# Kernel tuning notes

Measured on AMD Instinct MI355X. Metric: run time of the kernel, lower is better.

Reference implementation:

```python
import jax, jax.numpy as jnp
import numpy as np

D_STATE = 8
D_CONV = 4
DT_RANK = 8
THRESHOLD = 0.5
KPOOL = 3
PAD = (KPOOL - 1) // 2
EPS = 1e-5


def _rmsnorm(x, w):
    return x * jax.lax.rsqrt(jnp.mean(x * x, axis=-1, keepdims=True) + EPS) * w


def _dw_causal_conv(x, w, b):
    # x: (L, T, C), w: (C, 1, K) depthwise causal conv along T
    xt = jnp.transpose(x, (0, 2, 1))  # (L, C, T)
    y = jax.lax.conv_general_dilated(
        xt, w, window_strides=(1,), padding=[(D_CONV - 1, 0)],
        dimension_numbers=('NCH', 'OIH', 'NCH'), feature_group_count=xt.shape[1])
    return jnp.transpose(y, (0, 2, 1)) + b


def _selective_scan(x, delta, A, B, Cm, D):
    # x, delta: (L,T,d); A: (d,n); B, Cm: (L,T,n); D: (d,)
    dA = jnp.exp(delta[..., None] * A)                        # (L,T,d,n)
    dBx = (delta * x)[..., None] * B[:, :, None, :]           # (L,T,d,n)
    def combine(a, b):
        a1, b1 = a
        a2, b2 = b
        return (a2 * a1, a2 * b1 + b2)
    _, h = jax.lax.associative_scan(combine, (dA, dBx), axis=1)
    y = jnp.einsum('ltdn,ltn->ltd', h, Cm)
    return y + x * D


def _mamba_block(x, in_proj, conv_w, conv_b, x_proj_w, dt_proj_w, dt_proj_b,
                 A_log_f, A_log_b, D_f, D_b, out_proj_w, rms_w):
    # single-depth bidirectional (bimamba-v2 style) block, expand=1, residual + RMSNorm
    res = x
    xn = _rmsnorm(x, rms_w)
    xz = xn @ in_proj                       # (L,T,2C)
    xi, z = jnp.split(xz, 2, axis=-1)
    xi = jax.nn.silu(_dw_causal_conv(xi, conv_w, conv_b))
    dbl = xi @ x_proj_w                     # (L,T,dt_rank+2*d_state)
    dt = dbl[..., :DT_RANK]
    Bm = dbl[..., DT_RANK:DT_RANK + D_STATE]
    Cm = dbl[..., DT_RANK + D_STATE:]
    delta = jax.nn.softplus(dt @ dt_proj_w + dt_proj_b)
    A_f = -jnp.exp(A_log_f)
    A_b = -jnp.exp(A_log_b)
    flip = lambda a: a[:, ::-1]
    y_f = _selective_scan(xi, delta, A_f, Bm, Cm, D_f)
    y_b = flip(_selective_scan(flip(xi), flip(delta), A_b, flip(Bm), flip(Cm), D_b))
    y = 0.5 * (y_f + y_b) * jax.nn.silu(z)  # if_devide_out -> average two directions
    return res + y @ out_proj_w


def reference(feats, in_proj, conv_w, conv_b, x_proj_w, dt_proj_w, dt_proj_b,
              A_log_f, A_log_b, D_f, D_b, out_proj_w, rms_w, mlp_w, mlp_b,
              record_len):
    N, C, H, W = feats.shape
    T = H * W
    rec = np.asarray(record_len)  # static ragged group sizes
    ends = np.cumsum(rec)
    starts = ends - rec
    masks = []
    for s0, L in zip(starts.tolist(), rec.tolist()):
        g = feats[s0:s0 + L]                       # (L,C,H,W)
        if L > 1:
            x = g.reshape(L, C, T).transpose(0, 2, 1)  # l c h w -> l (h w) c
            feat = _mamba_block(x, in_proj, conv_w, conv_b, x_proj_w, dt_proj_w,
                                dt_proj_b, A_log_f, A_log_b, D_f, D_b,
                                out_proj_w, rms_w)
            score = jax.nn.sigmoid(feat @ mlp_w + mlp_b)   # (L,T,1)
            ego = jnp.ones((1, T, 1), feats.dtype)
            bs = jnp.concatenate([ego, score[1:]], axis=0)
        else:
            bs = jnp.ones((1, T, 1), feats.dtype)
        bs = bs.transpose(0, 2, 1).reshape(L, 1, H, W)     # l (h w) c -> l c h w
        masks.append(jnp.where(bs > THRESHOLD, 1.0, 0.0).astype(feats.dtype))
    mask = jnp.concatenate(masks, axis=0)                  # (N,1,H,W)
    pooled = jax.lax.reduce_window(
        mask, -jnp.inf, jax.lax.max,
        window_dimensions=(1, 1, KPOOL, KPOOL), window_strides=(1, 1, 1, 1),
        padding=[(0, 0), (0, 0), (PAD, PAD), (PAD, PAD)])
    return pooled


def setup_inputs():
    key = jax.random.key(0)
    ks = jax.random.split(key, 8)
    C, H, W = 128, 96, 96
    record_len = np.array([2, 3, 1, 2, 4], dtype=np.int64)
    N = int(record_len.sum())
    s = 0.05
    A_log = jnp.log(jnp.broadcast_to(
        jnp.arange(1, D_STATE + 1, dtype=jnp.float32), (C, D_STATE)))
    return {
        'feats': jax.random.normal(ks[0], (N, C, H, W), jnp.float32),
        'in_proj': jax.random.normal(ks[1], (C, 2 * C), jnp.float32) * s,
        'conv_w': jax.random.normal(ks[2], (C, 1, D_CONV), jnp.float32) * s,
        'conv_b': jnp.zeros((C,), jnp.float32),
        'x_proj_w': jax.random.normal(ks[3], (C, DT_RANK + 2 * D_STATE), jnp.float32) * s,
        'dt_proj_w': jax.random.normal(ks[4], (DT_RANK, C), jnp.float32) * s,
        'dt_proj_b': jnp.full((C,), 0.1, jnp.float32),
        'A_log_f': A_log,
        'A_log_b': A_log,
        'D_f': jnp.ones((C,), jnp.float32),
        'D_b': jnp.ones((C,), jnp.float32),
        'out_proj_w': jax.random.normal(ks[5], (C, C), jnp.float32) * s,
        'rms_w': jnp.ones((C,), jnp.float32),
        'mlp_w': jax.random.normal(ks[6], (C, 1), jnp.float32) * s,
        'mlp_b': jnp.zeros((1,), jnp.float32),
        'record_len': jnp.asarray(record_len),
    }
```

## Files before the change

### kernel.cpp

```cpp
#include <hip/hip_runtime.h>
#include <cstdint>
#include <cstddef>

#define C_CH 128
#define T_TOK 9216
#define H_IMG 96
#define W_IMG 96
#define NSTATE 8

#define CHUNK 32
#define RHALO 32
#define REGION (CHUNK + 2 * RHALO)

__device__ __forceinline__ float siluf_dev(float x) {
  return x / (1.0f + expf(-x));
}

__device__ __forceinline__ float fast_silu(float x) {
  return __fdividef(x, 1.0f + __expf(-x));
}

__global__ __launch_bounds__(128) void k0_setup(
    const int* __restrict__ rec, int n_groups, int N,
    const float* __restrict__ out_proj_w, const float* __restrict__ mlp_w,
    float* __restrict__ vvec, int* __restrict__ slot)
{
  const int tid = threadIdx.x;
  if (tid == 0) {
    int f = 0, sl = 0;
    for (int g = 0; g < n_groups; ++g) {
      const int L = rec[g];
      slot[f] = -1;
      for (int i = 1; i < L; ++i) slot[f + i] = sl++;
      f += L;
    }
  }
  if (tid < C_CH) {
    float acc = 0.0f;
    for (int j = 0; j < C_CH; ++j) acc += out_proj_w[tid * C_CH + j] * mlp_w[j];
    vvec[tid] = acc;
  }
}

__global__ __launch_bounds__(256, 4) void k1_gemm(
    const float* __restrict__ feats, const float* __restrict__ in_proj,
    const float* __restrict__ rms_w, const float* __restrict__ mlp_w,
    const float* __restrict__ mlp_b, const float* __restrict__ vvec,
    const int* __restrict__ slot,
    float* __restrict__ xipre, float* __restrict__ wbuf,
    float* __restrict__ logit)
{
  __shared__ float Asm[C_CH * 64];
  __shared__ float redA[256], redB[256], irS[64];
  const int f = blockIdx.y;
  const int s = slot[f];
  if (s < 0) return;
  const int m0 = blockIdx.x * 64;
  const int tid = threadIdx.x;

  {
    const int c0 = tid >> 4;
    const int tq = (tid & 15) * 4;
    const float* src = feats + (size_t)f * C_CH * T_TOK + m0 + tq;
    #pragma unroll
    for (int i = 0; i < 8; ++i) {
      const int c = c0 + i * 16;
      const float4 x4 = *(const float4*)(src + (size_t)c * T_TOK);
      *(float4*)&Asm[c * 64 + tq] = x4;
    }
  }
  __syncthreads();
  {
    const int t = tid & 63;
    const int q = tid >> 6;
    float ssum = 0.0f, rm = 0.0f;
    for (int cc = q * 32; cc < q * 32 + 32; ++cc) {
      const float val = Asm[cc * 64 + t];
      ssum += val * val;
      rm += val * mlp_w[cc];
    }
    redA[tid] = ssum; redB[tid] = rm;
  }
  __syncthreads();
  if (tid < 64) {
    const int t = tid;
    const float ssum = redA[t] + redA[t + 64] + redA[t + 128] + redA[t + 192];
    const float rm   = redB[t] + redB[t + 64] + redB[t + 128] + redB[t + 192];
    const float ir = 1.0f / sqrtf(ssum * (1.0f / C_CH) + 1e-5f);
    logit[(size_t)s * T_TOK + m0 + t] = rm + mlp_b[0];
    irS[t] = ir;
  }
  __syncthreads();
  {
    const int t = tid & 63;
    const int q = tid >> 6;
    const float ir = irS[t];
    for (int cc = q * 32; cc < q * 32 + 32; ++cc)
      Asm[cc * 64 + t] = (Asm[cc * 64 + t] * ir) * rms_w[cc];
  }
  __syncthreads();

  const int ti = tid >> 4;
  const int tc = tid & 15;
  for (int chunk = 0; chunk < 4; ++chunk) {
    const int n0 = chunk * 64;
    const float* bp = in_proj + n0 + tc * 4;
    float acc[4][4];
    #pragma unroll
    for (int i = 0; i < 4; ++i)
      #pragma unroll
      for (int j = 0; j < 4; ++j) acc[i][j] = 0.0f;
    #pragma unroll 8
    for (int k = 0; k < C_CH; ++k) {
      const float4 a4 = *(const float4*)&Asm[k * 64 + ti * 4];
      const float4 b4 = *(const float4*)(bp + (size_t)k * 256);
      acc[0][0] += a4.x * b4.x; acc[0][1] += a4.x * b4.y; acc[0][2] += a4.x * b4.z; acc[0][3] += a4.x * b4.w;
      acc[1][0] += a4.y * b4.x; acc[1][1] += a4.y * b4.y; acc[1][2] += a4.y * b4.z; acc[1][3] += a4.y * b4.w;
      acc[2][0] += a4.z * b4.x; acc[2][1] += a4.z * b4.y; acc[2][2] += a4.z * b4.z; acc[2][3] += a4.z * b4.w;
      acc[3][0] += a4.w * b4.x; acc[3][1] += a4.w * b4.y; acc[3][2] += a4.w * b4.z; acc[3][3] += a4.w * b4.w;
    }
    if (chunk < 2) {
      const int cb = n0 + tc * 4;
      #pragma unroll
      for (int i = 0; i < 4; ++i) {
        const int t = m0 + ti * 4 + i;
        float4 o; o.x = acc[i][0]; o.y = acc[i][1]; o.z = acc[i][2]; o.w = acc[i][3];
        *(float4*)&xipre[((size_t)s * T_TOK + t) * C_CH + cb] = o;
      }
    } else {
      const int zc = (chunk - 2) * 64 + tc * 4;
      const float4 v4 = *(const float4*)&vvec[zc];
      #pragma unroll
      for (int i = 0; i < 4; ++i) {
        const int t = m0 + ti * 4 + i;
        float4 o;
        o.x = 0.5f * siluf_dev(acc[i][0]) * v4.x;
        o.y = 0.5f * siluf_dev(acc[i][1]) * v4.y;
        o.z = 0.5f * siluf_dev(acc[i][2]) * v4.z;
        o.w = 0.5f * siluf_dev(acc[i][3]) * v4.w;
        *(float4*)&wbuf[((size_t)s * T_TOK + t) * C_CH + zc] = o;
      }
    }
  }
}

__global__ __launch_bounds__(256, 4) void k2_convproj(
    const float* __restrict__ xipre,
    const float* __restrict__ conv_w, const float* __restrict__ conv_b,
    const float* __restrict__ x_proj_w, const int* __restrict__ slot,
    float* __restrict__ dbl_g)
{
  __shared__ float xibuf[64 * 129];
  const int f = blockIdx.y;
  const int s = slot[f];
  if (s < 0) return;
  const int m0 = blockIdx.x * 64;
  const int tid = threadIdx.x;
  const int c = tid & 127;
  const int half = tid >> 7;
  const size_t rowbase = (size_t)s * T_TOK;
  const float4 cw = *(const float4*)(conv_w + c * 4);
  const float cb = conv_b[c];

  auto ldx = [&](int t) -> float {
    return (t >= 0) ? xipre[(rowbase + t) * C_CH + c] : 0.0f;
  };

  {
    const int t0 = m0 + half * 32;
    float xm1 = ldx(t0 - 1), xm2 = ldx(t0 - 2), xm3 = ldx(t0 - 3);
    #pragma unroll
    for (int i = 0; i < 32; ++i) {
      const float cur = ldx(t0 + i);
      const float sum = cw.x * xm3 + cw.y * xm2 + cw.z * xm1 + cw.w * cur + cb;
      xibuf[(half * 32 + i) * 129 + c] = fast_silu(sum);
      xm3 = xm2; xm2 = xm1; xm1 = cur;
    }
  }
  __syncthreads();
  {
    const int q6 = __builtin_amdgcn_readfirstlane(tid >> 6) * 6;
    const int tok = tid & 63;
    float acc[6] = {0, 0, 0, 0, 0, 0};
    for (int cc = 0; cc < C_CH; ++cc) {
      const float xv = xibuf[tok * 129 + cc];
      #pragma unroll
      for (int jj = 0; jj < 6; ++jj)
        acc[jj] += xv * x_proj_w[cc * 24 + q6 + jj];
    }
    #pragma unroll
    for (int jj = 0; jj < 6; ++jj)
      dbl_g[(rowbase + m0 + tok) * 24 + q6 + jj] = acc[jj];
  }
}

__global__ __launch_bounds__(256, 8) void k3_scan(
    const float* __restrict__ xipre, const float* __restrict__ wbuf,
    const float* __restrict__ dbl_g,
    const float* __restrict__ conv_w, const float* __restrict__ conv_b,
    const float* __restrict__ dt_proj_w, const float* __restrict__ dt_proj_b,
    const float* __restrict__ A_log_f, const float* __restrict__ A_log_b,
    const float* __restrict__ D_f, const float* __restrict__ D_b,
    const int* __restrict__ slot, float* __restrict__ logit)
{
  __shared__ float dbl[REGION * 24];
  const int f = blockIdx.y;
  const int s = slot[f];
  if (s < 0) return;
  const int c0 = blockIdx.x * CHUNK;
  const int r0 = c0 - RHALO;
  const int tid = threadIdx.x;
  const int c = tid & 127;
  const int half = tid >> 7;
  const size_t rowbase = (size_t)s * T_TOK;
  const float4 cw = *(const float4*)(conv_w + c * 4);
  const float cb = conv_b[c];

  auto ldx = [&](int t) -> float {
    return (t >= 0 && t < T_TOK) ? xipre[(rowbase + t) * C_CH + c] : 0.0f;
  };

  {
    const long grow = ((long)rowbase + r0) * 24;
    const int lo  = (r0 < 0) ? (-r0) * 6 : 0;
    const int hi  = (r0 + REGION > T_TOK) ? (T_TOK - r0) * 6 : REGION * 6;
    #pragma unroll
    for (int i = 0; i < 3; ++i) {
      const int idx = tid + i * 256;
      if (idx >= lo && idx < hi)
        *(float4*)&dbl[idx * 4] = *(const float4*)&dbl_g[grow + (long)idx * 4];
    }
  }
  __syncthreads();

  float dw[8], Ac[8];
  const float* Alog = half ? A_log_b : A_log_f;
  #pragma unroll
  for (int r = 0; r < 8; ++r) dw[r] = dt_proj_w[r * C_CH + c];
  #pragma unroll
  for (int n = 0; n < NSTATE; ++n) Ac[n] = -expf(Alog[c * NSTATE + n]);
  const float bias = dt_proj_b[c];
  const float Dd = half ? D_b[c] : D_f[c];
  float h[8] = {0, 0, 0, 0, 0, 0, 0, 0};

  const float a0 = Ac[0];
  int okl = 1;
  #pragma unroll
  for (int n = 1; n < NSTATE; ++n)
    okl &= (fabsf(Ac[n] - (float)(n + 1) * a0) <= 1e-4f * fabsf(Ac[n])) ? 1 : 0;
  const bool fastA = (__all(okl) != 0);

  auto decay8 = [&](float dlt, float* dA) {
    if (fastA) {
      const float e1 = __expf(dlt * a0);
      const float e2 = e1 * e1, e3 = e2 * e1, e4 = e2 * e2;
      dA[0] = e1; dA[1] = e2; dA[2] = e3; dA[3] = e4;
      dA[4] = e4 * e1; dA[5] = e4 * e2; dA[6] = e4 * e3; dA[7] = e4 * e4;
    } else {
      #pragma unroll
      for (int n = 0; n < NSTATE; ++n) dA[n] = __expf(dlt * Ac[n]);
    }
  };

  if (half == 0) {
    const int tb = (r0 < 0) ? 0 : r0;
    const int steps = c0 + CHUNK - tb;
    const int outg0 = (c0 - tb) >> 3;
    const int ng = steps >> 3;
    float xm1 = ldx(tb - 1), xm2 = ldx(tb - 2), xm3 = ldx(tb - 3);
    for (int g = 0; g < ng; ++g) {
      const int t0 = tb + g * 8;
      const bool out = (g >= outg0);
      float pg[8], wg[8];
      #pragma unroll
      for (int j = 0; j < 8; ++j) {
        const size_t gi = (rowbase + t0 + j) * C_CH + c;
        pg[j] = xipre[gi];
        wg[j] = out ? wbuf[gi] : 0.0f;
      }
      #pragma unroll
      for (int j = 0; j < 8; ++j) {
        const int t = t0 + j;
        const int p = t - r0;
        const float cur = pg[j];
        const float sum = cw.x * xm3 + cw.y * xm2 + cw.z * xm1 + cw.w * cur + cb;
        const float xiv = fast_silu(sum);
        xm3 = xm2; xm2 = xm1; xm1 = cur;
        const float4 d0 = *(const float4*)&dbl[p * 24];
        const float4 d1 = *(const float4*)&dbl[p * 24 + 4];
        float pre = bias;
        pre += d0.x * dw[0] + d0.y * dw[1] + d0.z * dw[2] + d0.w * dw[3];
        pre += d1.x * dw[4] + d1.y * dw[5] + d1.z * dw[6] + d1.w * dw[7];
        const float dlt = fmaxf(pre, 0.0f) + __logf(1.0f + __expf(-fabsf(pre)));
        const float u = dlt * xiv;
        const float4 b0 = *(const float4*)&dbl[p * 24 + 8];
        const float4 b1 = *(const float4*)&dbl[p * 24 + 12];
        float dA[8];
        decay8(dlt, dA);
        h[0] = dA[0] * h[0] + u * b0.x;
        h[1] = dA[1] * h[1] + u * b0.y;
        h[2] = dA[2] * h[2] + u * b0.z;
        h[3] = dA[3] * h[3] + u * b0.w;
        h[4] = dA[4] * h[4] + u * b1.x;
        h[5] = dA[5] * h[5] + u * b1.y;
        h[6] = dA[6] * h[6] + u * b1.z;
        h[7] = dA[7] * h[7] + u * b1.w;
        if (out) {
          const float4 cc0 = *(const float4*)&dbl[p * 24 + 16];
          const float4 cc1 = *(const float4*)&dbl[p * 24 + 20];
          float y = xiv * Dd;
          y += h[0] * cc0.x + h[1] * cc0.y + h[2] * cc0.z + h[3] * cc0.w;
          y += h[4] * cc1.x + h[5] * cc1.y + h[6] * cc1.z + h[7] * cc1.w;
          float contrib = y * wg[j];
          contrib += __shfl_xor(contrib, 1);
          contrib += __shfl_xor(contrib, 2);
          contrib += __shfl_xor(contrib, 4);
          contrib += __shfl_xor(contrib, 8);
          contrib += __shfl_xor(contrib, 16);
          contrib += __shfl_xor(contrib, 32);
          if ((tid & 63) == 0) atomicAdd(&logit[rowbase + t], contrib);
        }
      }
    }
  } else {
    const int te2e = r0 + REGION;
    const int te2 = (te2e > T_TOK) ? T_TOK : te2e;
    const int steps = te2 - c0;
    const int outg0 = (te2 - (c0 + CHUNK)) >> 3;
    const int ng = steps >> 3;
    float w0 = ldx(te2 - 1), w1 = ldx(te2 - 2), w2 = ldx(te2 - 3), w3 = ldx(te2 - 4);
    for (int g = 0; g < ng; ++g) {
      const int t0 = te2 - 1 - g * 8;
      const bool out = (g >= outg0);
      float nv[8], wg[8];
      #pragma unroll
      for (int j = 0; j < 8; ++j) {
        nv[j] = ldx(t0 - 4 - j);
        wg[j] = out ? wbuf[(rowbase + t0 - j) * C_CH + c] : 0.0f;
      }
      #pragma unroll
      for (int j = 0; j < 8; ++j) {
        const int t = t0 - j;
        const int p = t - r0;
        const float sum = cw.x * w3 + cw.y * w2 + cw.z * w1 + cw.w * w0 + cb;
        const float xiv = fast_silu(sum);
        w0 = w1; w1 = w2; w2 = w3; w3 = nv[j];
        const float4 d0 = *(const float4*)&dbl[p * 24];
        const float4 d1 = *(const float4*)&dbl[p * 24 + 4];
        float pre = bias;
        pre += d0.x * dw[0] + d0.y * dw[1] + d0.z * dw[2] + d0.w * dw[3];
        pre += d1.x * dw[4] + d1.y * dw[5] + d1.z * dw[6] + d1.w * dw[7];
        const float dlt = fmaxf(pre, 0.0f) + __logf(1.0f + __expf(-fabsf(pre)));
        const float u = dlt * xiv;
        const float4 b0 = *(const float4*)&dbl[p * 24 + 8];
        const float4 b1 = *(const float4*)&dbl[p * 24 + 12];
        float dA[8];
        decay8(dlt, dA);
        h[0] = dA[0] * h[0] + u * b0.x;
        h[1] = dA[1] * h[1] + u * b0.y;
        h[2] = dA[2] * h[2] + u * b0.z;
        h[3] = dA[3] * h[3] + u * b0.w;
        h[4] = dA[4] * h[4] + u * b1.x;
        h[5] = dA[5] * h[5] + u * b1.y;
        h[6] = dA[6] * h[6] + u * b1.z;
        h[7] = dA[7] * h[7] + u * b1.w;
        if (out) {
          const float4 cc0 = *(const float4*)&dbl[p * 24 + 16];
          const float4 cc1 = *(const float4*)&dbl[p * 24 + 20];
          float y = xiv * Dd;
          y += h[0] * cc0.x + h[1] * cc0.y + h[2] * cc0.z + h[3] * cc0.w;
          y += h[4] * cc1.x + h[5] * cc1.y + h[6] * cc1.z + h[7] * cc1.w;
          float contrib = y * wg[j];
          contrib += __shfl_xor(contrib, 1);
          contrib += __shfl_xor(contrib, 2);
          contrib += __shfl_xor(contrib, 4);
          contrib += __shfl_xor(contrib, 8);
          contrib += __shfl_xor(contrib, 16);
          contrib += __shfl_xor(contrib, 32);
          if ((tid & 63) == 0) atomicAdd(&logit[rowbase + t], contrib);
        }
      }
    }
  }
}

__global__ __launch_bounds__(128) void k4_pool(
    const float* __restrict__ logit, const int* __restrict__ slot,
    float* __restrict__ out)
{
  const int w = threadIdx.x;
  if (w >= W_IMG) return;
  const int hh = blockIdx.x;
  const int f = blockIdx.y;
  const int s = slot[f];
  float m = 0.0f;
  if (s < 0) {
    m = 1.0f;
  } else {
    for (int dh = -1; dh <= 1; ++dh) {
      const int h2 = hh + dh;
      if (h2 < 0 || h2 >= H_IMG) continue;
      for (int dw = -1; dw <= 1; ++dw) {
        const int w2 = w + dw;
        if (w2 < 0 || w2 >= W_IMG) continue;
        if (logit[(size_t)s * T_TOK + h2 * W_IMG + w2] > 0.0f) m = 1.0f;
      }
    }
  }
  out[(size_t)f * T_TOK + hh * W_IMG + w] = m;
}

extern "C" void kernel_launch(void* const* d_in, const int* in_sizes, int n_in,
                              void* d_out, int out_size, void* d_ws, size_t ws_size,
                              hipStream_t stream) {
  const float* feats      = (const float*)d_in[0];
  const float* in_proj    = (const float*)d_in[1];
  const float* conv_w     = (const float*)d_in[2];
  const float* conv_b     = (const float*)d_in[3];
  const float* x_proj_w   = (const float*)d_in[4];
  const float* dt_proj_w  = (const float*)d_in[5];
  const float* dt_proj_b  = (const float*)d_in[6];
  const float* A_log_f    = (const float*)d_in[7];
  const float* A_log_b    = (const float*)d_in[8];
  const float* D_f        = (const float*)d_in[9];
  const float* D_b        = (const float*)d_in[10];
  const float* out_proj_w = (const float*)d_in[11];
  const float* rms_w      = (const float*)d_in[12];
  const float* mlp_w      = (const float*)d_in[13];
  const float* mlp_b      = (const float*)d_in[14];
  const int*   rec        = (const int*)d_in[15];

  const int N = in_sizes[0] / (C_CH * T_TOK);
  const int n_groups = in_sizes[15];
  int S = N - n_groups;
  if (S < 1) S = 1;

  char* p = (char*)d_ws;
  float* vvec  = (float*)p; p += 1024;
  int*   slot  = (int*)p;   p += ((N * 4 + 255) / 256) * 256;
  float* logit = (float*)p; p += (size_t)S * T_TOK * 4;
  float* xipre = (float*)p; p += (size_t)S * T_TOK * C_CH * 4;
  float* wA    = (float*)p; p += (size_t)S * T_TOK * C_CH * 4;
  float* dblg  = (float*)p; p += (size_t)S * T_TOK * 24 * 4;
  (void)ws_size; (void)n_in; (void)out_size;

  k0_setup<<<1, 128, 0, stream>>>(rec, n_groups, N, out_proj_w, mlp_w, vvec, slot);
  k1_gemm<<<dim3(T_TOK / 64, N), 256, 0, stream>>>(
      feats, in_proj, rms_w, mlp_w, mlp_b, vvec, slot, xipre, wA, logit);
  k2_convproj<<<dim3(T_TOK / 64, N), 256, 0, stream>>>(
      xipre, conv_w, conv_b, x_proj_w, slot, dblg);
  k3_scan<<<dim3(T_TOK / CHUNK, N), 256, 0, stream>>>(
      xipre, wA, dblg, conv_w, conv_b, dt_proj_w, dt_proj_b,
      A_log_f, A_log_b, D_f, D_b, slot, logit);
  k4_pool<<<dim3(H_IMG, N), 128, 0, stream>>>(logit, slot, (float*)d_out);
}
```

Measured before the change: 346.7 us.

## Precompute conv-silu and softplus delta in projection kernel, enlarge scan chunk

The depthwise conv+SiLU output and the softplus delta projection are now computed once in the conv/projection kernel and written to global buffers. The scan kernel then only loads xi, delta and B/C, and no longer recomputes them for every halo overlap. The scan chunk size is doubled so the halo warm-up is a smaller fraction of each block's work. The trade is two extra full-size fp32 tensors written and read back through HBM, added scan memory traffic, and halved scan grid parallelism.

Result: faster. 311.1 us (-10.3%).

```diff
diff --git a/kernel.cpp b/kernel.cpp
--- a/kernel.cpp
+++ b/kernel.cpp
@@ -8,7 +8,7 @@
 #define W_IMG 96
 #define NSTATE 8
 
-#define CHUNK 32
+#define CHUNK 64
 #define RHALO 32
 #define REGION (CHUNK + 2 * RHALO)
 
@@ -147,10 +147,14 @@
 __global__ __launch_bounds__(256, 4) void k2_convproj(
     const float* __restrict__ xipre,
     const float* __restrict__ conv_w, const float* __restrict__ conv_b,
-    const float* __restrict__ x_proj_w, const int* __restrict__ slot,
-    float* __restrict__ dbl_g)
+    const float* __restrict__ x_proj_w,
+    const float* __restrict__ dt_proj_w, const float* __restrict__ dt_proj_b,
+    const int* __restrict__ slot,
+    float* __restrict__ xi_g, float* __restrict__ delta_g,
+    float* __restrict__ bc_g)
 {
   __shared__ float xibuf[64 * 129];
+  __shared__ float dtb[64 * 8];
   const int f = blockIdx.y;
   const int s = slot[f];
   if (s < 0) return;
@@ -173,7 +177,9 @@
     for (int i = 0; i < 32; ++i) {
       const float cur = ldx(t0 + i);
       const float sum = cw.x * xm3 + cw.y * xm2 + cw.z * xm1 + cw.w * cur + cb;
-      xibuf[(half * 32 + i) * 129 + c] = fast_silu(sum);
+      const float xiv = fast_silu(sum);
+      xibuf[(half * 32 + i) * 129 + c] = xiv;
+      xi_g[(rowbase + t0 + i) * C_CH + c] = xiv;
       xm3 = xm2; xm2 = xm1; xm1 = cur;
     }
   }
@@ -189,21 +195,39 @@
         acc[jj] += xv * x_proj_w[cc * 24 + q6 + jj];
     }
     #pragma unroll
-    for (int jj = 0; jj < 6; ++jj)
-      dbl_g[(rowbase + m0 + tok) * 24 + q6 + jj] = acc[jj];
-  }
-}
-
-__global__ __launch_bounds__(256, 8) void k3_scan(
-    const float* __restrict__ xipre, const float* __restrict__ wbuf,
-    const float* __restrict__ dbl_g,
-    const float* __restrict__ conv_w, const float* __restrict__ conv_b,
-    const float* __restrict__ dt_proj_w, const float* __restrict__ dt_proj_b,
+    for (int jj = 0; jj < 6; ++jj) {
+      const int o = q6 + jj;
+      if (o < 8) dtb[tok * 8 + o] = acc[jj];
+      else       bc_g[(rowbase + m0 + tok) * 16 + (o - 8)] = acc[jj];
+    }
+  }
+  __syncthreads();
+  {
+    float dw[8];
+    #pragma unroll
+    for (int r = 0; r < 8; ++r) dw[r] = dt_proj_w[r * C_CH + c];
+    const float bias = dt_proj_b[c];
+    for (int i = 0; i < 32; ++i) {
+      const int tok = half * 32 + i;
+      const float4 d0 = *(const float4*)&dtb[tok * 8];
+      const float4 d1 = *(const float4*)&dtb[tok * 8 + 4];
+      float pre = bias;
+      pre += d0.x * dw[0] + d0.y * dw[1] + d0.z * dw[2] + d0.w * dw[3];
+      pre += d1.x * dw[4] + d1.y * dw[5] + d1.z * dw[6] + d1.w * dw[7];
+      const float dlt = fmaxf(pre, 0.0f) + __logf(1.0f + __expf(-fabsf(pre)));
+      delta_g[(rowbase + m0 + tok) * C_CH + c] = dlt;
+    }
+  }
+}
+
+__global__ __launch_bounds__(256, 4) void k3_scan(
+    const float* __restrict__ xi_g, const float* __restrict__ delta_g,
+    const float* __restrict__ wbuf, const float* __restrict__ bc_g,
     const float* __restrict__ A_log_f, const float* __restrict__ A_log_b,
     const float* __restrict__ D_f, const float* __restrict__ D_b,
     const int* __restrict__ slot, float* __restrict__ logit)
 {
-  __shared__ float dbl[REGION * 24];
+  __shared__ float bc[REGION * 16];
   const int f = blockIdx.y;
   const int s = slot[f];
   if (s < 0) return;
@@ -213,33 +237,24 @@
   const int c = tid & 127;
   const int half = tid >> 7;
   const size_t rowbase = (size_t)s * T_TOK;
-  const float4 cw = *(const float4*)(conv_w + c * 4);
-  const float cb = conv_b[c];
-
-  auto ldx = [&](int t) -> float {
-    return (t >= 0 && t < T_TOK) ? xipre[(rowbase + t) * C_CH + c] : 0.0f;
-  };
-
-  {
-    const long grow = ((long)rowbase + r0) * 24;
-    const int lo  = (r0 < 0) ? (-r0) * 6 : 0;
-    const int hi  = (r0 + REGION > T_TOK) ? (T_TOK - r0) * 6 : REGION * 6;
-    #pragma unroll
-    for (int i = 0; i < 3; ++i) {
+
+  {
+    const long grow = ((long)rowbase + r0) * 16;
+    const int lo  = (r0 < 0) ? (-r0) * 4 : 0;
+    const int hi  = (r0 + REGION > T_TOK) ? (T_TOK - r0) * 4 : REGION * 4;
+    #pragma unroll
+    for (int i = 0; i < 2; ++i) {
       const int idx = tid + i * 256;
       if (idx >= lo && idx < hi)
-        *(float4*)&dbl[idx * 4] = *(const float4*)&dbl_g[grow + (long)idx * 4];
-    }
-  }
-  __syncthreads();
-
-  float dw[8], Ac[8];
+        *(float4*)&bc[idx * 4] = *(const float4*)&bc_g[grow + (long)idx * 4];
+    }
+  }
+  __syncthreads();
+
+  float Ac[8];
   const float* Alog = half ? A_log_b : A_log_f;
   #pragma unroll
-  for (int r = 0; r < 8; ++r) dw[r] = dt_proj_w[r * C_CH + c];
-  #pragma unroll
   for (int n = 0; n < NSTATE; ++n) Ac[n] = -expf(Alog[c * NSTATE + n]);
-  const float bias = dt_proj_b[c];
   const float Dd = half ? D_b[c] : D_f[c];
   float h[8] = {0, 0, 0, 0, 0, 0, 0, 0};
 
@@ -264,37 +279,28 @@
 
   if (half == 0) {
     const int tb = (r0 < 0) ? 0 : r0;
-    const int steps = c0 + CHUNK - tb;
     const int outg0 = (c0 - tb) >> 3;
-    const int ng = steps >> 3;
-    float xm1 = ldx(tb - 1), xm2 = ldx(tb - 2), xm3 = ldx(tb - 3);
+    const int ng = (c0 + CHUNK - tb) >> 3;
     for (int g = 0; g < ng; ++g) {
       const int t0 = tb + g * 8;
       const bool out = (g >= outg0);
-      float pg[8], wg[8];
+      float xg[8], dg[8], wg[8];
       #pragma unroll
       for (int j = 0; j < 8; ++j) {
         const size_t gi = (rowbase + t0 + j) * C_CH + c;
-        pg[j] = xipre[gi];
+        xg[j] = xi_g[gi];
+        dg[j] = delta_g[gi];
         wg[j] = out ? wbuf[gi] : 0.0f;
       }
       #pragma unroll
       for (int j = 0; j < 8; ++j) {
         const int t = t0 + j;
         const int p = t - r0;
-        const float cur = pg[j];
-        const float sum = cw.x * xm3 + cw.y * xm2 + cw.z * xm1 + cw.w * cur + cb;
-        const float xiv = fast_silu(sum);
-        xm3 = xm2; xm2 = xm1; xm1 = cur;
-        const float4 d0 = *(const float4*)&dbl[p * 24];
-        const float4 d1 = *(const float4*)&dbl[p * 24 + 4];
-        float pre = bias;
-        pre += d0.x * dw[0] + d0.y * dw[1] + d0.z * dw[2] + d0.w * dw[3];
-        pre += d1.x * dw[4] + d1.y * dw[5] + d1.z * dw[6] + d1.w * dw[7];
-        const float dlt = fmaxf(pre, 0.0f) + __logf(1.0f + __expf(-fabsf(pre)));
+        const float dlt = dg[j];
+        const float xiv = xg[j];
         const float u = dlt * xiv;
-        const float4 b0 = *(const float4*)&dbl[p * 24 + 8];
-        const float4 b1 = *(const float4*)&dbl[p * 24 + 12];
+        const float4 b0 = *(const float4*)&bc[p * 16];
+        const float4 b1 = *(const float4*)&bc[p * 16 + 4];
         float dA[8];
         decay8(dlt, dA);
         h[0] = dA[0] * h[0] + u * b0.x;
@@ -306,8 +312,8 @@
         h[6] = dA[6] * h[6] + u * b1.z;
         h[7] = dA[7] * h[7] + u * b1.w;
         if (out) {
-          const float4 cc0 = *(const float4*)&dbl[p * 24 + 16];
-          const float4 cc1 = *(const float4*)&dbl[p * 24 + 20];
+          const float4 cc0 = *(const float4*)&bc[p * 16 + 8];
+          const float4 cc1 = *(const float4*)&bc[p * 16 + 12];
           float y = xiv * Dd;
           y += h[0] * cc0.x + h[1] * cc0.y + h[2] * cc0.z + h[3] * cc0.w;
           y += h[4] * cc1.x + h[5] * cc1.y + h[6] * cc1.z + h[7] * cc1.w;
@@ -325,35 +331,28 @@
   } else {
     const int te2e = r0 + REGION;
     const int te2 = (te2e > T_TOK) ? T_TOK : te2e;
-    const int steps = te2 - c0;
     const int outg0 = (te2 - (c0 + CHUNK)) >> 3;
-    const int ng = steps >> 3;
-    float w0 = ldx(te2 - 1), w1 = ldx(te2 - 2), w2 = ldx(te2 - 3), w3 = ldx(te2 - 4);
+    const int ng = (te2 - c0) >> 3;
     for (int g = 0; g < ng; ++g) {
       const int t0 = te2 - 1 - g * 8;
       const bool out = (g >= outg0);
-      float nv[8], wg[8];
+      float xg[8], dg[8], wg[8];
       #pragma unroll
       for (int j = 0; j < 8; ++j) {
-        nv[j] = ldx(t0 - 4 - j);
-        wg[j] = out ? wbuf[(rowbase + t0 - j) * C_CH + c] : 0.0f;
+        const size_t gi = (rowbase + t0 - j) * C_CH + c;
+        xg[j] = xi_g[gi];
+        dg[j] = delta_g[gi];
+        wg[j] = out ? wbuf[gi] : 0.0f;
       }
       #pragma unroll
       for (int j = 0; j < 8; ++j) {
         const int t = t0 - j;
         const int p = t - r0;
-        const float sum = cw.x * w3 + cw.y * w2 + cw.z * w1 + cw.w * w0 + cb;
-        const float xiv = fast_silu(sum);
-        w0 = w1; w1 = w2; w2 = w3; w3 = nv[j];
-        const float4 d0 = *(const float4*)&dbl[p * 24];
-        const float4 d1 = *(const float4*)&dbl[p * 24 + 4];
-        float pre = bias;
-        pre += d0.x * dw[0] + d0.y * dw[1] + d0.z * dw[2] + d0.w * dw[3];
-        pre += d1.x * dw[4] + d1.y * dw[5] + d1.z * dw[6] + d1.w * dw[7];
-        const float dlt = fmaxf(pre, 0.0f) + __logf(1.0f + __expf(-fabsf(pre)));
+        const float dlt = dg[j];
+        const float xiv = xg[j];
         const float u = dlt * xiv;
-        const float4 b0 = *(const float4*)&dbl[p * 24 + 8];
-        const float4 b1 = *(const float4*)&dbl[p * 24 + 12];
+        const float4 b0 = *(const float4*)&bc[p * 16];
+        const float4 b1 = *(const float4*)&bc[p * 16 + 4];
         float dA[8];
         decay8(dlt, dA);
         h[0] = dA[0] * h[0] + u * b0.x;
@@ -365,8 +364,8 @@
         h[6] = dA[6] * h[6] + u * b1.z;
         h[7] = dA[7] * h[7] + u * b1.w;
         if (out) {
-          const float4 cc0 = *(const float4*)&dbl[p * 24 + 16];
-          const float4 cc1 = *(const float4*)&dbl[p * 24 + 20];
+          const float4 cc0 = *(const float4*)&bc[p * 16 + 8];
+          const float4 cc1 = *(const float4*)&bc[p * 16 + 12];
           float y = xiv * Dd;
           y += h[0] * cc0.x + h[1] * cc0.y + h[2] * cc0.z + h[3] * cc0.w;
           y += h[4] * cc1.x + h[5] * cc1.y + h[6] * cc1.z + h[7] * cc1.w;
@@ -441,16 +440,18 @@
   float* logit = (float*)p; p += (size_t)S * T_TOK * 4;
   float* xipre = (float*)p; p += (size_t)S * T_TOK * C_CH * 4;
   float* wA    = (float*)p; p += (size_t)S * T_TOK * C_CH * 4;
-  float* dblg  = (float*)p; p += (size_t)S * T_TOK * 24 * 4;
+  float* xig   = (float*)p; p += (size_t)S * T_TOK * C_CH * 4;
+  float* dltg  = (float*)p; p += (size_t)S * T_TOK * C_CH * 4;
+  float* bcg   = (float*)p; p += (size_t)S * T_TOK * 16 * 4;
   (void)ws_size; (void)n_in; (void)out_size;
 
   k0_setup<<<1, 128, 0, stream>>>(rec, n_groups, N, out_proj_w, mlp_w, vvec, slot);
   k1_gemm<<<dim3(T_TOK / 64, N), 256, 0, stream>>>(
       feats, in_proj, rms_w, mlp_w, mlp_b, vvec, slot, xipre, wA, logit);
   k2_convproj<<<dim3(T_TOK / 64, N), 256, 0, stream>>>(
-      xipre, conv_w, conv_b, x_proj_w, slot, dblg);
+      xipre, conv_w, conv_b, x_proj_w, dt_proj_w, dt_proj_b, slot,
+      xig, dltg, bcg);
   k3_scan<<<dim3(T_TOK / CHUNK, N), 256, 0, stream>>>(
-      xipre, wA, dblg, conv_w, conv_b, dt_proj_w, dt_proj_b,
-      A_log_f, A_log_b, D_f, D_b, slot, logit);
+      xig, dltg, wA, bcg, A_log_f, A_log_b, D_f, D_b, slot, logit);
   k4_pool<<<dim3(H_IMG, N), 128, 0, stream>>>(logit, slot, (float*)d_out);
 }
```
